# Optimization experiments

Hardware: AMD Instinct MI355X
Metric: run time of the kernel (lower is better)

The kernel has to match this reference:

```python
import jax, jax.numpy as jnp
import numpy as np

N, C_IN, C_OUT, HID, H = 4096, 512, 512, 128, 4
HEAD_OUT = C_OUT // H  # 128
MID = 4 * C_OUT        # 2048
R = 1.0                # spatial radius r
L = 48                 # sequence window l
NEG = -1e9


def layer_norm(x, g, b, eps=1e-5):
    m = jnp.mean(x, axis=-1, keepdims=True)
    v = jnp.mean(jnp.square(x - m), axis=-1, keepdims=True)
    return (x - m) * jax.lax.rsqrt(v + eps) * g + b


def setup_inputs() -> dict:
    key = jax.random.key(0)
    ks = jax.random.split(key, 16)
    s = lambda fan: 1.0 / np.sqrt(fan)
    return {
        "x":   jax.random.normal(ks[0], (N, C_IN), jnp.float32),
        "pos": jax.random.normal(ks[1], (N, 3), jnp.float32),
        "ori": jax.random.normal(ks[2], (N, 3), jnp.float32),
        "seq": jnp.arange(N, dtype=jnp.int64) if jax.config.jax_enable_x64 else jnp.arange(N, dtype=jnp.int32),
        "batch": jnp.sort(jax.random.randint(ks[3], (N,), 0, 8)),
        "ln1_g": jnp.ones((C_IN,), jnp.float32),
        "ln1_b": jnp.zeros((C_IN,), jnp.float32),
        "ln2_g": jnp.ones((C_OUT,), jnp.float32),
        "ln2_b": jnp.zeros((C_OUT,), jnp.float32),
        "Wq": jax.random.normal(ks[4], (H, C_IN, HID), jnp.float32) * s(C_IN),
        "Wk": jax.random.normal(ks[5], (H, C_IN, HID), jnp.float32) * s(C_IN),
        "Wv": jax.random.normal(ks[6], (H, C_IN, HID), jnp.float32) * s(C_IN),
        "Wo": jax.random.normal(ks[7], (H, HID, HEAD_OUT), jnp.float32) * s(HID),
        "lnm_g": jnp.ones((MID,), jnp.float32),
        "lnm_b": jnp.zeros((MID,), jnp.float32),
        "W1": jax.random.normal(ks[8], (C_OUT, MID), jnp.float32) * s(C_OUT),
        "W2": jax.random.normal(ks[9], (MID, C_OUT), jnp.float32) * s(MID),
    }


def _block(x, pos, ori, seq, batch, ln1_g, ln1_b, ln2_g, ln2_b,
           Wq, Wk, Wv, Wo, lnm_g, lnm_b, W1, W2):
    identity = x
    xn = layer_norm(x, ln1_g, ln1_b)

    # geometry/sequence neighborhood mask: same graph, ||dp||<=r, |ds|<=l
    d2 = jnp.sum(jnp.square(pos[:, None, :] - pos[None, :, :]), axis=-1)  # [N,N]
    ds = jnp.abs(seq[:, None] - seq[None, :])
    mask = (batch[:, None] == batch[None, :]) & (d2 <= R * R) & (ds <= L)

    # all heads at once (original loops over heads; math identical)
    q = jnp.einsum('nc,hcd->hnd', xn, Wq)
    k = jnp.einsum('nc,hcd->hnd', xn, Wk)
    v = jnp.einsum('nc,hcd->hnd', xn, Wv)
    gbias = ori @ ori.T  # geometric orientation bias [N,N]
    scores = jnp.einsum('hnd,hmd->hnm', q, k) / np.sqrt(HID) + gbias[None]
    scores = jnp.where(mask[None], scores, NEG)
    attn = jax.nn.softmax(scores, axis=-1)
    o = jnp.einsum('hnm,hmd->hnd', attn, v)
    o = jnp.einsum('hnd,hde->hne', o, Wo)               # [H,N,HEAD_OUT]
    o = jnp.transpose(o, (1, 0, 2)).reshape(N, C_OUT)   # concat heads

    x = o + identity
    identity = x
    h = layer_norm(x, ln2_g, ln2_b) @ W1
    h = jax.nn.relu(layer_norm(h, lnm_g, lnm_b))
    return h @ W2 + identity


def reference(x, pos, ori, seq, batch, ln1_g, ln1_b, ln2_g, ln2_b,
              Wq, Wk, Wv, Wo, lnm_g, lnm_b, W1, W2):
    return _block(x, pos, ori, seq, batch, ln1_g, ln1_b, ln2_g, ln2_b,
                  Wq, Wk, Wv, Wo, lnm_g, lnm_b, W1, W2)
```

## Files before the change

### kernel.cpp

```cpp
#include <hip/hip_runtime.h>

typedef unsigned short u16;
typedef unsigned int u32;
typedef float f32x4 __attribute__((ext_vector_type(4)));
typedef __bf16 bf16x8 __attribute__((ext_vector_type(8)));

#define N_TOK 4096
#define QKV_LD 1536
#define NH 4
#define HID 128
#define C_OUT 512

__device__ __forceinline__ float b2f(u16 u) { return __uint_as_float(((u32)u) << 16); }
__device__ __forceinline__ u16 f2b(float f) {
  u32 u = __float_as_uint(f);
  u32 r = (u + 0x7fffu + ((u >> 16) & 1u)) >> 16;
  return (u16)r;
}

__device__ __forceinline__ void gload16(const u16* g, u16* l) {
  __builtin_amdgcn_global_load_lds(
      (const __attribute__((address_space(1))) void*)g,
      (__attribute__((address_space(3))) void*)l, 16, 0, 0);
}

__device__ __forceinline__ void tr32(const float* __restrict__ s,
                                     u16* __restrict__ d, int R, int C,
                                     int r0, int c0, u16 (*tile)[33]) {
  const int tx = threadIdx.x & 31, ty = threadIdx.x >> 5;
#pragma unroll
  for (int i = 0; i < 32; i += 8)
    tile[ty + i][tx] = f2b(s[(size_t)(r0 + ty + i) * C + c0 + tx]);
  __syncthreads();
#pragma unroll
  for (int i = 0; i < 32; i += 8)
    d[(size_t)(c0 + ty + i) * R + r0 + tx] = tile[tx][ty + i];
}

__device__ __forceinline__ void ln512_body(
    const float* __restrict__ x, const float* __restrict__ g,
    const float* __restrict__ b, u16* __restrict__ y, int row) {
  const int lane = threadIdx.x & 63;
  const float* xr = x + (size_t)row * 512;
  const int c = lane * 8;
  float4 a0 = *(const float4*)(xr + c);
  float4 a1 = *(const float4*)(xr + c + 4);
  float v[8] = {a0.x, a0.y, a0.z, a0.w, a1.x, a1.y, a1.z, a1.w};
  float s1 = 0.f, s2 = 0.f;
#pragma unroll
  for (int i = 0; i < 8; i++) { s1 += v[i]; s2 += v[i] * v[i]; }
#pragma unroll
  for (int o = 32; o; o >>= 1) { s1 += __shfl_xor(s1, o); s2 += __shfl_xor(s2, o); }
  float mean = s1 * (1.f / 512.f);
  float var = s2 * (1.f / 512.f) - mean * mean;
  float rs = rsqrtf(fmaxf(var, 0.f) + 1e-5f);
  float4 g0 = *(const float4*)(g + c), g1 = *(const float4*)(g + c + 4);
  float4 b0 = *(const float4*)(b + c), b1 = *(const float4*)(b + c + 4);
  float gg[8] = {g0.x, g0.y, g0.z, g0.w, g1.x, g1.y, g1.z, g1.w};
  float bb[8] = {b0.x, b0.y, b0.z, b0.w, b1.x, b1.y, b1.z, b1.w};
  u16 t[8];
#pragma unroll
  for (int i = 0; i < 8; i++) t[i] = f2b((v[i] - mean) * rs * gg[i] + bb[i]);
  *(uint4*)(y + (size_t)row * 512 + c) = *(const uint4*)t;
}

__global__ __launch_bounds__(256) void prep(
    const float* __restrict__ x, const float* __restrict__ ln1g,
    const float* __restrict__ ln1b, u16* __restrict__ xn,
    const float* __restrict__ Wq, const float* __restrict__ Wk,
    const float* __restrict__ Wv, const float* __restrict__ Wo,
    const float* __restrict__ W1,
    u16* __restrict__ Btqkv, u16* __restrict__ Wot, u16* __restrict__ W1t)
{
  __shared__ u16 tile[32][33];
  const int bid = blockIdx.x;
  if (bid < 1024) {
    ln512_body(x, ln1g, ln1b, xn, bid * 4 + (threadIdx.x >> 6));
    return;
  }
  const int idx = bid - 1024;
  const float* s; u16* d; int R, C, r0, c0;
  if (idx < 1024) {
    s = W1; d = W1t; R = 512; C = 2048;
    r0 = (idx >> 6) * 32; c0 = (idx & 63) * 32;
  } else if (idx < 1792) {
    int i = idx - 1024;
    int z = i >> 6, rem = i & 63;
    int which = z >> 2, b = z & 3;
    const float* base = (which == 0) ? Wq : (which == 1) ? Wk : Wv;
    s = base + (size_t)b * 512 * 128;
    d = Btqkv + (size_t)which * 4 * 512 * 128 + (size_t)b * 512 * 128;
    R = 512; C = 128;
    r0 = (rem >> 2) * 32; c0 = (rem & 3) * 32;
  } else {
    int i = idx - 1792;
    int b = i >> 4, rem = i & 15;
    s = Wo + (size_t)b * 128 * 128;
    d = Wot + (size_t)b * 128 * 128;
    R = 128; C = 128;
    r0 = (rem >> 2) * 32; c0 = (rem & 3) * 32;
  }
  tr32(s, d, R, C, r0, c0, tile);
}

__global__ __launch_bounds__(256) void ln512_f32(
    const float* __restrict__ x, const float* __restrict__ g,
    const float* __restrict__ b, u16* __restrict__ y)
{
  ln512_body(x, g, b, y, blockIdx.x * 4 + (threadIdx.x >> 6));
}

__global__ __launch_bounds__(256) void ln2048_bf16_relu(
    const u16* __restrict__ x, const float* __restrict__ g,
    const float* __restrict__ b, u16* __restrict__ y)
{
  const int row = blockIdx.x, tid = threadIdx.x;
  const int c = tid * 8;
  const u16* xr = x + (size_t)row * 2048;
  uint4 u = *(const uint4*)(xr + c);
  u16 e[8]; *(uint4*)e = u;
  float v[8];
#pragma unroll
  for (int i = 0; i < 8; i++) v[i] = b2f(e[i]);
  float s1 = 0.f, s2 = 0.f;
#pragma unroll
  for (int i = 0; i < 8; i++) { s1 += v[i]; s2 += v[i] * v[i]; }
#pragma unroll
  for (int o = 32; o; o >>= 1) { s1 += __shfl_xor(s1, o); s2 += __shfl_xor(s2, o); }
  __shared__ float red[2][4];
  int lane = tid & 63, w = tid >> 6;
  if (lane == 0) { red[0][w] = s1; red[1][w] = s2; }
  __syncthreads();
  s1 = red[0][0] + red[0][1] + red[0][2] + red[0][3];
  s2 = red[1][0] + red[1][1] + red[1][2] + red[1][3];
  float mean = s1 * (1.f / 2048.f);
  float var = s2 * (1.f / 2048.f) - mean * mean;
  float rs = rsqrtf(fmaxf(var, 0.f) + 1e-5f);
  float4 g0 = *(const float4*)(g + c), g1 = *(const float4*)(g + c + 4);
  float4 b0 = *(const float4*)(b + c), b1 = *(const float4*)(b + c + 4);
  float gg[8] = {g0.x, g0.y, g0.z, g0.w, g1.x, g1.y, g1.z, g1.w};
  float bb[8] = {b0.x, b0.y, b0.z, b0.w, b1.x, b1.y, b1.z, b1.w};
  u16 t[8];
#pragma unroll
  for (int i = 0; i < 8; i++)
    t[i] = f2b(fmaxf((v[i] - mean) * rs * gg[i] + bb[i], 0.f));
  *(uint4*)(y + (size_t)row * 2048 + c) = *(const uint4*)t;
}

__global__ __launch_bounds__(512, 4) void gemm128(
    const u16* __restrict__ A, int lda,
    const u16* __restrict__ Bt,
    void* __restrict__ C, int ldc, int outf32,
    const float* __restrict__ res,
    int Kslice, int Ktot, int atomic)
{
  __shared__ u16 As[2][128 * 64];
  __shared__ u16 Bs[2][128 * 64];
  const int id = blockIdx.x + gridDim.x * blockIdx.y;
  const int xr = id & 7, xj = id >> 3;
  const int bm = xr * 4 + (xj & 3);
  const int bn = xj >> 2;
  const int m0 = bm * 128, n0 = bn * 128;
  const int kbase = blockIdx.z * Kslice;
  const int tid = threadIdx.x;
  const int lane = tid & 63, w = tid >> 6;
  const int wm = (w & 1) * 64;
  const int wn = (w >> 1) * 32;
  const int l16 = lane & 15, quad = lane >> 4;

  const int sr = tid >> 3;
  const int sch = (tid & 7) ^ (sr & 7);
  const u16* PA = A + (size_t)(m0 + sr) * lda + kbase + sch * 8;
  const u16* PB = Bt + (size_t)(n0 + sr) * Ktot + kbase + sch * 8;
  const size_t askip = (size_t)64 * lda;
  const size_t bskip = (size_t)64 * Ktot;

  f32x4 acc[4][2];
#pragma unroll
  for (int i = 0; i < 4; i++)
#pragma unroll
    for (int j = 0; j < 2; j++) acc[i][j] = (f32x4){0.f, 0.f, 0.f, 0.f};

  {
    gload16(PA, &As[0][w * 512]);
    gload16(PA + askip, &As[0][4096 + w * 512]);
    gload16(PB, &Bs[0][w * 512]);
    gload16(PB + bskip, &Bs[0][4096 + w * 512]);
  }
  __syncthreads();

  int buf = 0;
  for (int kk = 0; kk < Kslice; kk += 64) {
    if (kk + 64 < Kslice) {
      PA += 64; PB += 64;
      gload16(PA, &As[buf ^ 1][w * 512]);
      gload16(PA + askip, &As[buf ^ 1][4096 + w * 512]);
      gload16(PB, &Bs[buf ^ 1][w * 512]);
      gload16(PB + bskip, &Bs[buf ^ 1][4096 + w * 512]);
    }
#pragma unroll
    for (int kc = 0; kc < 2; kc++) {
      bf16x8 af[4], bfr[2];
#pragma unroll
      for (int mt = 0; mt < 4; mt++) {
        int row = wm + mt * 16 + l16;
        af[mt] = *(const bf16x8*)&As[buf][row * 64 + (((kc * 4 + quad) ^ (row & 7)) * 8)];
      }
#pragma unroll
      for (int nt = 0; nt < 2; nt++) {
        int row = wn + nt * 16 + l16;
        bfr[nt] = *(const bf16x8*)&Bs[buf][row * 64 + (((kc * 4 + quad) ^ (row & 7)) * 8)];
      }
#pragma unroll
      for (int mt = 0; mt < 4; mt++)
#pragma unroll
        for (int nt = 0; nt < 2; nt++)
          acc[mt][nt] = __builtin_amdgcn_mfma_f32_16x16x32_bf16(
              af[mt], bfr[nt], acc[mt][nt], 0, 0, 0);
    }
    __syncthreads();
    buf ^= 1;
  }

#pragma unroll
  for (int mt = 0; mt < 4; mt++)
#pragma unroll
    for (int nt = 0; nt < 2; nt++)
#pragma unroll
      for (int r = 0; r < 4; r++) {
        int gr = m0 + wm + mt * 16 + quad * 4 + r;
        int gc = n0 + wn + nt * 16 + l16;
        size_t off = (size_t)gr * ldc + gc;
        float v = acc[mt][nt][r];
        if (atomic) {
          atomicAdd((float*)C + off, v);
        } else {
          if (res) v += res[off];
          if (outf32) ((float*)C)[off] = v;
          else        ((u16*)C)[off] = f2b(v);
        }
      }
}

#define TQ 16
#define BAND 112
#define KROW 136
#define PROW 120
__global__ __launch_bounds__(256) void attn_mfma(
    const u16* __restrict__ qkv, const float* __restrict__ pos,
    const float* __restrict__ ori, const int* __restrict__ batch,
    const u16* __restrict__ wot, const float* __restrict__ xres,
    float* __restrict__ out,
    const float* __restrict__ W2, u16* __restrict__ W2t)
{
  __shared__ u16 kv[128 * KROW];
  __shared__ u16 qp[TQ * KROW];
  __shared__ float ps[TQ * PROW];
  __shared__ float bpx[BAND], bpy[BAND], bpz[BAND];
  __shared__ float box_[BAND], boy_[BAND], boz_[BAND];
  __shared__ int bb[BAND];

  if (blockIdx.x >= 256) {
    int idx = (blockIdx.x - 256) + blockIdx.y * 256;
    int r0 = (idx >> 4) * 32, c0 = (idx & 15) * 32;
    tr32(W2, W2t, 2048, 512, r0, c0, (u16(*)[33])kv);
    return;
  }

  const int h = blockIdx.y;
  const int bxs = (blockIdx.x & 7) * 32 + (blockIdx.x >> 3);
  const int i0 = bxs * TQ;
  const int j0 = i0 - 48;
  const int tid = threadIdx.x;
  const int lane = tid & 63, w = tid >> 6;
  const int l16 = lane & 15, quad = lane >> 4;

  for (int t = tid; t < BAND; t += 256) {
    int j = j0 + t;
    if (j >= 0 && j < N_TOK) {
      bpx[t] = pos[j * 3 + 0]; bpy[t] = pos[j * 3 + 1]; bpz[t] = pos[j * 3 + 2];
      box_[t] = ori[j * 3 + 0]; boy_[t] = ori[j * 3 + 1]; boz_[t] = ori[j * 3 + 2];
      bb[t] = batch[j];
    } else {
      bpx[t] = bpy[t] = bpz[t] = 0.f;
      box_[t] = boy_[t] = boz_[t] = 0.f;
      bb[t] = -12345;
    }
  }
  for (int idx = tid; idx < BAND * 16; idx += 256) {
    int t = idx >> 4, c8 = (idx & 15) * 8;
    int j = j0 + t;
    int4 val = {0, 0, 0, 0};
    if (j >= 0 && j < N_TOK)
      val = *(const int4*)&qkv[(size_t)j * QKV_LD + 512 + h * HID + c8];
    *(int4*)&kv[t * KROW + c8] = val;
  }
  {
    int q = tid >> 4, c8 = (tid & 15) * 8;
    *(int4*)&qp[q * KROW + c8] =
        *(const int4*)&qkv[(size_t)(i0 + q) * QKV_LD + h * HID + c8];
  }
  __syncthreads();

  {
    bf16x8 af[4];
#pragma unroll
    for (int kc = 0; kc < 4; kc++)
      af[kc] = *(const bf16x8*)&qp[l16 * KROW + kc * 32 + quad * 8];
#pragma unroll
    for (int ti = 0; ti < 2; ti++) {
      int tt = w + ti * 4;
      if (tt < 7) {
        f32x4 acc = (f32x4){0.f, 0.f, 0.f, 0.f};
#pragma unroll
        for (int kc = 0; kc < 4; kc++) {
          bf16x8 bf = *(const bf16x8*)&kv[(tt * 16 + l16) * KROW + kc * 32 + quad * 8];
          acc = __builtin_amdgcn_mfma_f32_16x16x32_bf16(af[kc], bf, acc, 0, 0, 0);
        }
        int t = tt * 16 + l16;
#pragma unroll
        for (int r = 0; r < 4; r++) {
          int q = quad * 4 + r, iq = q + 48;
          int dseq = iq - t;
          bool ok = (bb[t] == bb[iq]) && (dseq <= 48) && (dseq >= -48);
          {
#pragma clang fp contract(off)
            float dx = bpx[iq] - bpx[t], dy = bpy[iq] - bpy[t], dz = bpz[iq] - bpz[t];
            float d2 = dx * dx + dy * dy + dz * dz;
            ok = ok && (d2 <= 1.0f);
          }
          float s = -1e9f;
          if (ok) {
            float gb = box_[iq] * box_[t] + boy_[iq] * boy_[t] + boz_[iq] * boz_[t];
            s = acc[r] * 0.08838834764831845f + gb;
          }
          ps[q * PROW + t] = s;
        }
      }
    }
  }
  __syncthreads();

  for (int idx = tid; idx < BAND * 32; idx += 256) {
    int t = idx >> 5, d4 = (idx & 31) * 4;
    int j = j0 + t;
    uint2 val; val.x = 0; val.y = 0;
    if (j >= 0 && j < N_TOK)
      val = *(const uint2*)&qkv[(size_t)j * QKV_LD + 1024 + h * HID + d4];
    u16 e[4] = {(u16)val.x, (u16)(val.x >> 16), (u16)val.y, (u16)(val.y >> 16)};
#pragma unroll
    for (int jj = 0; jj < 4; jj++) {
      int dd = (jj + tid) & 3;
      kv[(d4 + dd) * KROW + t] = e[dd];
    }
  }
  for (int idx = tid; idx < 128 * 16; idx += 256) {
    int d = idx >> 4, t = BAND + (idx & 15);
    kv[d * KROW + t] = 0;
  }
  {
    int row = tid >> 4, sub = tid & 15;
    float vals[7];
    float m = -1e30f;
#pragma unroll
    for (int i = 0; i < 7; i++) {
      vals[i] = ps[row * PROW + sub + i * 16];
      m = fmaxf(m, vals[i]);
    }
#pragma unroll
    for (int o = 8; o; o >>= 1) m = fmaxf(m, __shfl_xor(m, o));
    float s = 0.f;
#pragma unroll
    for (int i = 0; i < 7; i++) { vals[i] = __expf(vals[i] - m); s += vals[i]; }
#pragma unroll
    for (int o = 8; o; o >>= 1) s += __shfl_xor(s, o);
    float inv = 1.f / s;
#pragma unroll
    for (int i = 0; i < 7; i++)
      qp[row * KROW + sub + i * 16] = f2b(vals[i] * inv);
    qp[row * KROW + BAND + sub] = 0;
  }
  __syncthreads();

  u16 obuf[2][4];
  {
    bf16x8 paf[4];
#pragma unroll
    for (int kc = 0; kc < 4; kc++)
      paf[kc] = *(const bf16x8*)&qp[l16 * KROW + kc * 32 + quad * 8];
#pragma unroll
    for (int ti = 0; ti < 2; ti++) {
      int dt = w + ti * 4;
      f32x4 acc = (f32x4){0.f, 0.f, 0.f, 0.f};
#pragma unroll
      for (int kc = 0; kc < 4; kc++) {
        bf16x8 bf = *(const bf16x8*)&kv[(dt * 16 + l16) * KROW + kc * 32 + quad * 8];
        acc = __builtin_amdgcn_mfma_f32_16x16x32_bf16(paf[kc], bf, acc, 0, 0, 0);
      }
#pragma unroll
      for (int r = 0; r < 4; r++) obuf[ti][r] = f2b(acc[r]);
    }
  }
  __syncthreads();

#pragma unroll
  for (int ti = 0; ti < 2; ti++) {
    int dt = w + ti * 4;
#pragma unroll
    for (int r = 0; r < 4; r++)
      qp[(quad * 4 + r) * KROW + dt * 16 + l16] = obuf[ti][r];
  }
  {
    const u16* wsrc = wot + (size_t)h * HID * HID;
    for (int idx = tid; idx < 128 * 16; idx += 256) {
      int e = idx >> 4, c8 = (idx & 15) * 8;
      *(int4*)&kv[e * KROW + c8] = *(const int4*)&wsrc[e * HID + c8];
    }
  }
  __syncthreads();

  {
    bf16x8 oaf[4];
#pragma unroll
    for (int kc = 0; kc < 4; kc++)
      oaf[kc] = *(const bf16x8*)&qp[l16 * KROW + kc * 32 + quad * 8];
#pragma unroll
    for (int ti = 0; ti < 2; ti++) {
      int et = w + ti * 4;
      f32x4 acc = (f32x4){0.f, 0.f, 0.f, 0.f};
#pragma unroll
      for (int kc = 0; kc < 4; kc++) {
        bf16x8 bf = *(const bf16x8*)&kv[(et * 16 + l16) * KROW + kc * 32 + quad * 8];
        acc = __builtin_amdgcn_mfma_f32_16x16x32_bf16(oaf[kc], bf, acc, 0, 0, 0);
      }
#pragma unroll
      for (int r = 0; r < 4; r++) {
        int q = quad * 4 + r;
        size_t off = (size_t)(i0 + q) * C_OUT + h * HID + et * 16 + l16;
        out[off] = acc[r] + xres[off];
      }
    }
  }
}

#define MB (1048576)
extern "C" void kernel_launch(void* const* d_in, const int* in_sizes, int n_in,
                              void* d_out, int out_size, void* d_ws, size_t ws_size,
                              hipStream_t stream) {
  const float* x    = (const float*)d_in[0];
  const float* pos  = (const float*)d_in[1];
  const float* ori  = (const float*)d_in[2];
  const int*   batch = (const int*)d_in[4];
  const float* ln1g = (const float*)d_in[5];
  const float* ln1b = (const float*)d_in[6];
  const float* ln2g = (const float*)d_in[7];
  const float* ln2b = (const float*)d_in[8];
  const float* Wq = (const float*)d_in[9];
  const float* Wk = (const float*)d_in[10];
  const float* Wv = (const float*)d_in[11];
  const float* Wo = (const float*)d_in[12];
  const float* lnmg = (const float*)d_in[13];
  const float* lnmb = (const float*)d_in[14];
  const float* W1 = (const float*)d_in[15];
  const float* W2 = (const float*)d_in[16];
  float* out = (float*)d_out;

  char* ws = (char*)d_ws;
  u16* xn    = (u16*)(ws + 0);
  u16* x1n   = (u16*)(ws + 0);
  u16* qkv   = (u16*)(ws + 4 * MB);
  u16* h     = (u16*)(ws + 4 * MB);
  u16* Wot   = (u16*)(ws + 16 * MB);
  u16* Btqkv = (u16*)(ws + 20 * MB);
  u16* W2t   = (u16*)(ws + 20 * MB);
  u16* W1t   = (u16*)(ws + 22 * MB);

  prep<<<dim3(2880), 256, 0, stream>>>(x, ln1g, ln1b, xn,
                                       Wq, Wk, Wv, Wo, W1, Btqkv, Wot, W1t);
  gemm128<<<dim3(12, 32, 1), 512, 0, stream>>>(xn, 512, Btqkv, qkv, QKV_LD, 0,
                                               nullptr, 512, 512, 0);
  attn_mfma<<<dim3(512, NH), 256, 0, stream>>>(qkv, pos, ori, batch, Wot, x, out,
                                               W2, W2t);
  ln512_f32<<<dim3(1024), 256, 0, stream>>>(out, ln2g, ln2b, x1n);
  gemm128<<<dim3(16, 32, 1), 512, 0, stream>>>(x1n, 512, W1t, h, 2048, 0,
                                               nullptr, 512, 512, 0);
  ln2048_bf16_relu<<<dim3(4096), 256, 0, stream>>>(h, lnmg, lnmb, h);
  gemm128<<<dim3(4, 32, 2), 512, 0, stream>>>(h, 2048, W2t, out, 512, 1,
                                              nullptr, 1024, 2048, 1);
}
```

Before: 191.6 us.

## Double attention query tile to 32 rows with 512-thread blocks and 8 waves

```diff
diff --git a/kernel.cpp b/kernel.cpp
--- a/kernel.cpp
+++ b/kernel.cpp
@@ -34,6 +34,19 @@
   __syncthreads();
 #pragma unroll
   for (int i = 0; i < 32; i += 8)
+    d[(size_t)(c0 + ty + i) * R + r0 + tx] = tile[tx][ty + i];
+}
+
+__device__ __forceinline__ void tr32_512(const float* __restrict__ s,
+                                         u16* __restrict__ d, int R, int C,
+                                         int r0, int c0, u16 (*tile)[33]) {
+  const int tx = threadIdx.x & 31, ty = threadIdx.x >> 5;
+#pragma unroll
+  for (int i = 0; i < 32; i += 16)
+    tile[ty + i][tx] = f2b(s[(size_t)(r0 + ty + i) * C + c0 + tx]);
+  __syncthreads();
+#pragma unroll
+  for (int i = 0; i < 32; i += 16)
     d[(size_t)(c0 + ty + i) * R + r0 + tx] = tile[tx][ty + i];
 }
 
@@ -242,11 +255,11 @@
       }
 }
 
-#define TQ 16
-#define BAND 112
+#define TQ 32
+#define BAND 128
 #define KROW 136
-#define PROW 120
-__global__ __launch_bounds__(256) void attn_mfma(
+#define PROW 132
+__global__ __launch_bounds__(512) void attn_mfma(
     const u16* __restrict__ qkv, const float* __restrict__ pos,
     const float* __restrict__ ori, const int* __restrict__ batch,
     const u16* __restrict__ wot, const float* __restrict__ xres,
@@ -260,23 +273,23 @@
   __shared__ float box_[BAND], boy_[BAND], boz_[BAND];
   __shared__ int bb[BAND];
 
-  if (blockIdx.x >= 256) {
-    int idx = (blockIdx.x - 256) + blockIdx.y * 256;
+  if (blockIdx.x >= 128) {
+    int idx = (blockIdx.x - 128) + blockIdx.y * 256;
     int r0 = (idx >> 4) * 32, c0 = (idx & 15) * 32;
-    tr32(W2, W2t, 2048, 512, r0, c0, (u16(*)[33])kv);
+    tr32_512(W2, W2t, 2048, 512, r0, c0, (u16(*)[33])kv);
     return;
   }
 
   const int h = blockIdx.y;
-  const int bxs = (blockIdx.x & 7) * 32 + (blockIdx.x >> 3);
+  const int bxs = (blockIdx.x & 7) * 16 + (blockIdx.x >> 3);
   const int i0 = bxs * TQ;
   const int j0 = i0 - 48;
   const int tid = threadIdx.x;
   const int lane = tid & 63, w = tid >> 6;
   const int l16 = lane & 15, quad = lane >> 4;
 
-  for (int t = tid; t < BAND; t += 256) {
-    int j = j0 + t;
+  if (tid < BAND) {
+    int t = tid, j = j0 + t;
     if (j >= 0 && j < N_TOK) {
       bpx[t] = pos[j * 3 + 0]; bpy[t] = pos[j * 3 + 1]; bpz[t] = pos[j * 3 + 2];
       box_[t] = ori[j * 3 + 0]; boy_[t] = ori[j * 3 + 1]; boz_[t] = ori[j * 3 + 2];
@@ -287,7 +300,7 @@
       bb[t] = -12345;
     }
   }
-  for (int idx = tid; idx < BAND * 16; idx += 256) {
+  for (int idx = tid; idx < BAND * 16; idx += 512) {
     int t = idx >> 4, c8 = (idx & 15) * 8;
     int j = j0 + t;
     int4 val = {0, 0, 0, 0};
@@ -303,45 +316,44 @@
   __syncthreads();
 
   {
-    bf16x8 af[4];
+    bf16x8 bf[4];
 #pragma unroll
     for (int kc = 0; kc < 4; kc++)
-      af[kc] = *(const bf16x8*)&qp[l16 * KROW + kc * 32 + quad * 8];
-#pragma unroll
-    for (int ti = 0; ti < 2; ti++) {
-      int tt = w + ti * 4;
-      if (tt < 7) {
-        f32x4 acc = (f32x4){0.f, 0.f, 0.f, 0.f};
-#pragma unroll
-        for (int kc = 0; kc < 4; kc++) {
-          bf16x8 bf = *(const bf16x8*)&kv[(tt * 16 + l16) * KROW + kc * 32 + quad * 8];
-          acc = __builtin_amdgcn_mfma_f32_16x16x32_bf16(af[kc], bf, acc, 0, 0, 0);
+      bf[kc] = *(const bf16x8*)&kv[(w * 16 + l16) * KROW + kc * 32 + quad * 8];
+    const int t = w * 16 + l16;
+#pragma unroll
+    for (int qt = 0; qt < 2; qt++) {
+      bf16x8 af[4];
+#pragma unroll
+      for (int kc = 0; kc < 4; kc++)
+        af[kc] = *(const bf16x8*)&qp[(qt * 16 + l16) * KROW + kc * 32 + quad * 8];
+      f32x4 acc = (f32x4){0.f, 0.f, 0.f, 0.f};
+#pragma unroll
+      for (int kc = 0; kc < 4; kc++)
+        acc = __builtin_amdgcn_mfma_f32_16x16x32_bf16(af[kc], bf[kc], acc, 0, 0, 0);
+#pragma unroll
+      for (int r = 0; r < 4; r++) {
+        int q = qt * 16 + quad * 4 + r, iq = q + 48;
+        int dseq = iq - t;
+        bool ok = (bb[t] == bb[iq]) && (dseq <= 48) && (dseq >= -48);
+        {
+#pragma clang fp contract(off)
+          float dx = bpx[iq] - bpx[t], dy = bpy[iq] - bpy[t], dz = bpz[iq] - bpz[t];
+          float d2 = dx * dx + dy * dy + dz * dz;
+          ok = ok && (d2 <= 1.0f);
         }
-        int t = tt * 16 + l16;
-#pragma unroll
-        for (int r = 0; r < 4; r++) {
-          int q = quad * 4 + r, iq = q + 48;
-          int dseq = iq - t;
-          bool ok = (bb[t] == bb[iq]) && (dseq <= 48) && (dseq >= -48);
-          {
-#pragma clang fp contract(off)
-            float dx = bpx[iq] - bpx[t], dy = bpy[iq] - bpy[t], dz = bpz[iq] - bpz[t];
-            float d2 = dx * dx + dy * dy + dz * dz;
-            ok = ok && (d2 <= 1.0f);
-          }
-          float s = -1e9f;
-          if (ok) {
-            float gb = box_[iq] * box_[t] + boy_[iq] * boy_[t] + boz_[iq] * boz_[t];
-            s = acc[r] * 0.08838834764831845f + gb;
-          }
-          ps[q * PROW + t] = s;
+        float s = -1e9f;
+        if (ok) {
+          float gb = box_[iq] * box_[t] + boy_[iq] * boy_[t] + boz_[iq] * boz_[t];
+          s = acc[r] * 0.08838834764831845f + gb;
         }
+        ps[q * PROW + t] = s;
       }
     }
   }
   __syncthreads();
 
-  for (int idx = tid; idx < BAND * 32; idx += 256) {
+  for (int idx = tid; idx < BAND * 32; idx += 512) {
     int t = idx >> 5, d4 = (idx & 31) * 4;
     int j = j0 + t;
     uint2 val; val.x = 0; val.y = 0;
@@ -354,16 +366,12 @@
       kv[(d4 + dd) * KROW + t] = e[dd];
     }
   }
-  for (int idx = tid; idx < 128 * 16; idx += 256) {
-    int d = idx >> 4, t = BAND + (idx & 15);
-    kv[d * KROW + t] = 0;
-  }
   {
     int row = tid >> 4, sub = tid & 15;
-    float vals[7];
+    float vals[8];
     float m = -1e30f;
 #pragma unroll
-    for (int i = 0; i < 7; i++) {
+    for (int i = 0; i < 8; i++) {
       vals[i] = ps[row * PROW + sub + i * 16];
       m = fmaxf(m, vals[i]);
     }
@@ -371,48 +379,47 @@
     for (int o = 8; o; o >>= 1) m = fmaxf(m, __shfl_xor(m, o));
     float s = 0.f;
 #pragma unroll
-    for (int i = 0; i < 7; i++) { vals[i] = __expf(vals[i] - m); s += vals[i]; }
+    for (int i = 0; i < 8; i++) { vals[i] = __expf(vals[i] - m); s += vals[i]; }
 #pragma unroll
     for (int o = 8; o; o >>= 1) s += __shfl_xor(s, o);
     float inv = 1.f / s;
 #pragma unroll
-    for (int i = 0; i < 7; i++)
+    for (int i = 0; i < 8; i++)
       qp[row * KROW + sub + i * 16] = f2b(vals[i] * inv);
-    qp[row * KROW + BAND + sub] = 0;
   }
   __syncthreads();
 
   u16 obuf[2][4];
   {
-    bf16x8 paf[4];
+    bf16x8 bf[4];
 #pragma unroll
     for (int kc = 0; kc < 4; kc++)
-      paf[kc] = *(const bf16x8*)&qp[l16 * KROW + kc * 32 + quad * 8];
-#pragma unroll
-    for (int ti = 0; ti < 2; ti++) {
-      int dt = w + ti * 4;
+      bf[kc] = *(const bf16x8*)&kv[(w * 16 + l16) * KROW + kc * 32 + quad * 8];
+#pragma unroll
+    for (int qt = 0; qt < 2; qt++) {
+      bf16x8 paf[4];
+#pragma unroll
+      for (int kc = 0; kc < 4; kc++)
+        paf[kc] = *(const bf16x8*)&qp[(qt * 16 + l16) * KROW + kc * 32 + quad * 8];
       f32x4 acc = (f32x4){0.f, 0.f, 0.f, 0.f};
 #pragma unroll
-      for (int kc = 0; kc < 4; kc++) {
-        bf16x8 bf = *(const bf16x8*)&kv[(dt * 16 + l16) * KROW + kc * 32 + quad * 8];
-        acc = __builtin_amdgcn_mfma_f32_16x16x32_bf16(paf[kc], bf, acc, 0, 0, 0);
-      }
-#pragma unroll
-      for (int r = 0; r < 4; r++) obuf[ti][r] = f2b(acc[r]);
-    }
-  }
-  __syncthreads();
-
-#pragma unroll
-  for (int ti = 0; ti < 2; ti++) {
-    int dt = w + ti * 4;
+      for (int kc = 0; kc < 4; kc++)
+        acc = __builtin_amdgcn_mfma_f32_16x16x32_bf16(paf[kc], bf[kc], acc, 0, 0, 0);
+#pragma unroll
+      for (int r = 0; r < 4; r++) obuf[qt][r] = f2b(acc[r]);
+    }
+  }
+  __syncthreads();
+
+#pragma unroll
+  for (int qt = 0; qt < 2; qt++) {
 #pragma unroll
     for (int r = 0; r < 4; r++)
-      qp[(quad * 4 + r) * KROW + dt * 16 + l16] = obuf[ti][r];
+      qp[(qt * 16 + quad * 4 + r) * KROW + w * 16 + l16] = obuf[qt][r];
   }
   {
     const u16* wsrc = wot + (size_t)h * HID * HID;
-    for (int idx = tid; idx < 128 * 16; idx += 256) {
+    for (int idx = tid; idx < 128 * 16; idx += 512) {
       int e = idx >> 4, c8 = (idx & 15) * 8;
       *(int4*)&kv[e * KROW + c8] = *(const int4*)&wsrc[e * HID + c8];
     }
@@ -420,23 +427,24 @@
   __syncthreads();
 
   {
-    bf16x8 oaf[4];
+    bf16x8 bf[4];
 #pragma unroll
     for (int kc = 0; kc < 4; kc++)
-      oaf[kc] = *(const bf16x8*)&qp[l16 * KROW + kc * 32 + quad * 8];
-#pragma unroll
-    for (int ti = 0; ti < 2; ti++) {
-      int et = w + ti * 4;
+      bf[kc] = *(const bf16x8*)&kv[(w * 16 + l16) * KROW + kc * 32 + quad * 8];
+#pragma unroll
+    for (int qt = 0; qt < 2; qt++) {
+      bf16x8 oaf[4];
+#pragma unroll
+      for (int kc = 0; kc < 4; kc++)
+        oaf[kc] = *(const bf16x8*)&qp[(qt * 16 + l16) * KROW + kc * 32 + quad * 8];
       f32x4 acc = (f32x4){0.f, 0.f, 0.f, 0.f};
 #pragma unroll
-      for (int kc = 0; kc < 4; kc++) {
-        bf16x8 bf = *(const bf16x8*)&kv[(et * 16 + l16) * KROW + kc * 32 + quad * 8];
-        acc = __builtin_amdgcn_mfma_f32_16x16x32_bf16(oaf[kc], bf, acc, 0, 0, 0);
-      }
+      for (int kc = 0; kc < 4; kc++)
+        acc = __builtin_amdgcn_mfma_f32_16x16x32_bf16(oaf[kc], bf[kc], acc, 0, 0, 0);
 #pragma unroll
       for (int r = 0; r < 4; r++) {
-        int q = quad * 4 + r;
-        size_t off = (size_t)(i0 + q) * C_OUT + h * HID + et * 16 + l16;
+        int q = qt * 16 + quad * 4 + r;
+        size_t off = (size_t)(i0 + q) * C_OUT + h * HID + w * 16 + l16;
         out[off] = acc[r] + xres[off];
       }
     }
@@ -479,7 +487,7 @@
                                        Wq, Wk, Wv, Wo, W1, Btqkv, Wot, W1t);
   gemm128<<<dim3(12, 32, 1), 512, 0, stream>>>(xn, 512, Btqkv, qkv, QKV_LD, 0,
                                                nullptr, 512, 512, 0);
-  attn_mfma<<<dim3(512, NH), 256, 0, stream>>>(qkv, pos, ori, batch, Wot, x, out,
+  attn_mfma<<<dim3(384, NH), 512, 0, stream>>>(qkv, pos, ori, batch, Wot, x, out,
                                                W2, W2t);
   ln512_f32<<<dim3(1024), 256, 0, stream>>>(out, ln2g, ln2b, x1n);
   gemm128<<<dim3(16, 32, 1), 512, 0, stream>>>(x1n, 512, W1t, h, 2048, 0,
```

Measured after the change: 182.2 us. 4.9% less time.
